# Kernel optimization log

Hardware: AMD Instinct MI355X
Metric: run time of the kernel (lower is better)

The kernel has to match this reference:

```python
import jax, jax.numpy as jnp
import numpy as np

B, T_ENC, FEAT, H, W2V, T_DEC, V = 32, 80, 4096, 256, 256, 30, 32000


def lstm_cell(x, h, c, w_ih, w_hh, b_ih, b_hh):
    # PyTorch LSTMCell: gates order i, f, g, o
    g = x @ w_ih.T + h @ w_hh.T + b_ih + b_hh
    i, f, gg, o = jnp.split(g, 4, axis=-1)
    c_new = jax.nn.sigmoid(f) * c + jax.nn.sigmoid(i) * jnp.tanh(gg)
    h_new = jax.nn.sigmoid(o) * jnp.tanh(c_new)
    return h_new, c_new


def setup_inputs() -> dict:
    key = jax.random.key(0)
    ks = jax.random.split(key, 13)
    s = 0.05
    return {
        'feat': jax.random.normal(ks[0], (B, T_ENC, FEAT), jnp.float32),
        'caption': jax.random.normal(ks[1], (B, T_DEC, W2V), jnp.float32),
        'caption_one_hot': jax.random.normal(ks[2], (B, T_DEC, V), jnp.float32),
        'keep_rate': 1,
        'w_ih1': jax.random.normal(ks[3], (4 * H, FEAT), jnp.float32) * s,
        'w_hh1': jax.random.normal(ks[4], (4 * H, H), jnp.float32) * s,
        'b_ih1': jax.random.normal(ks[5], (4 * H,), jnp.float32) * s,
        'b_hh1': jax.random.normal(ks[6], (4 * H,), jnp.float32) * s,
        'w_ih2': jax.random.normal(ks[7], (4 * H, H + W2V), jnp.float32) * s,
        'w_hh2': jax.random.normal(ks[8], (4 * H, H), jnp.float32) * s,
        'b_ih2': jax.random.normal(ks[9], (4 * H,), jnp.float32) * s,
        'b_hh2': jax.random.normal(ks[10], (4 * H,), jnp.float32) * s,
        'w_out': jax.random.normal(ks[11], (V, H), jnp.float32) * s,
        'b_out': jax.random.normal(ks[12], (V,), jnp.float32) * s,
    }


def reference(feat, caption, caption_one_hot, keep_rate,
              w_ih1, w_hh1, b_ih1, b_hh1,
              w_ih2, w_hh2, b_ih2, b_hh2,
              w_out, b_out):
    zeros_h = jnp.zeros((B, H), feat.dtype)
    pad1 = jnp.zeros((B, FEAT), feat.dtype)

    # ---------------- encoder: 80 steps ----------------
    def enc_step(carry, x_t):
        h1, c1, h2, c2 = carry
        h1, c1 = lstm_cell(x_t, h1, c1, w_ih1, w_hh1, b_ih1, b_hh1)
        h2, c2 = lstm_cell(jnp.concatenate([zeros_h, h1], axis=1), h2, c2,
                           w_ih2, w_hh2, b_ih2, b_hh2)
        return (h1, c1, h2, c2), h2

    (h1, c1, h2, c2), enc_h2 = jax.lax.scan(
        enc_step, (zeros_h, zeros_h, zeros_h, zeros_h),
        jnp.transpose(feat, (1, 0, 2)))
    enc_h2 = jnp.transpose(enc_h2, (1, 0, 2))  # [B, 80, H]

    # ---------------- decoder: teacher forcing (coin>=100 never fires) ----
    targets = jnp.argmax(caption_one_hot, axis=-1)  # [B, T_DEC]

    def dec_step(carry, xs):
        h1, c1, h2, c2, loss = carry
        word_t, tgt_t = xs  # [B, W2V], [B]
        h1, c1 = lstm_cell(pad1, h1, c1, w_ih1, w_hh1, b_ih1, b_hh1)
        h2n, c2 = lstm_cell(jnp.concatenate([word_t, h1], axis=1), h2, c2,
                            w_ih2, w_hh2, b_ih2, b_hh2)
        logits = h2n @ w_out.T + b_out  # [B, V]
        logp = jax.nn.log_softmax(logits, axis=-1)
        ce = -jnp.take_along_axis(logp, tgt_t[:, None], axis=1)[:, 0]
        loss = loss + jnp.mean(ce) / B  # sum(mean-CE)/batch, per original
        # attention: scores of encoder h2 states against current h2
        attn = jax.nn.softmax(jnp.einsum('bsh,bh->bs', enc_h2, h2n), axis=-1)
        ctx = jnp.einsum('bs,bsh->bh', attn, enc_h2)  # replaces h2 for next step
        return (h1, c1, ctx, c2, loss), None

    xs = (jnp.transpose(caption[:, :T_DEC - 1, :], (1, 0, 2)),
          jnp.transpose(targets[:, 1:T_DEC], (1, 0)))
    (h1, c1, h2, c2, total_loss), _ = jax.lax.scan(
        dec_step, (h1, c1, h2, c2, jnp.float32(0.0)), xs)
    return total_loss
```

## Files before the change

kernel.cpp:

```cpp
#include <hip/hip_runtime.h>
#include <hip/hip_bf16.h>
#include <math.h>

#define BB 32
#define TE 80
#define FEAT 4096
#define HH 256
#define W2V 256
#define TD 30
#define VV 32000
#define G4 1024

typedef unsigned short u16;
typedef unsigned int u32;
using f32x4 = __attribute__((ext_vector_type(4))) float;
using bf16x8 = __attribute__((ext_vector_type(8))) short;
using f16x2 = __attribute__((ext_vector_type(2))) _Float16;

#define SENT 0xFFFFFFFFu

__device__ __forceinline__ float sigm(float x) { return 1.0f / (1.0f + expf(-x)); }
__device__ __forceinline__ u16 f2bf(float f) {
  u32 u = __float_as_uint(f);
  u32 r = (u + 0x7FFFu + ((u >> 16) & 1u)) >> 16;
  return (u16)r;
}
__device__ __forceinline__ u32 packh2(float lo, float hi) {
  f16x2 v = {(_Float16)lo, (_Float16)hi};
  return __builtin_bit_cast(u32, v);
}

#define AT_LOAD(p)     __hip_atomic_load((p), __ATOMIC_RELAXED, __HIP_MEMORY_SCOPE_AGENT)
#define AT_STORE(p, v) __hip_atomic_store((p), (v), __ATOMIC_RELAXED, __HIP_MEMORY_SCOPE_AGENT)

__device__ __forceinline__ float fdot2h(f16x2 a, f16x2 b, float c) {
#if __has_builtin(__builtin_amdgcn_fdot2)
  return __builtin_amdgcn_fdot2(a, b, c, false);
#else
  return c + (float)a[0] * (float)b[0] + (float)a[1] * (float)b[1];
#endif
}

__global__ __launch_bounds__(256) void prep_kernel(
    const float* __restrict__ w_ih1, const float* __restrict__ w_out,
    const float* __restrict__ w_ih2, const float* __restrict__ caption,
    const float* __restrict__ onehot,
    const float* __restrict__ b_ih1, const float* __restrict__ b_hh1,
    const float* __restrict__ b_ih2, const float* __restrict__ b_hh2,
    u16* __restrict__ w_ih1b, u16* __restrict__ wPK,
    u16* __restrict__ w_ih2lb, u16* __restrict__ capb,
    float* __restrict__ bias1, float* __restrict__ bias2,
    u32* __restrict__ H1H, u32* __restrict__ H2H,
    float* __restrict__ loss, int* __restrict__ cectr,
    int* __restrict__ targets) {
  int blk = blockIdx.x, tid = threadIdx.x;
  if (blk < 4096) {
    int i = blk * 256 + tid;
    float4 v = *(const float4*)&w_ih1[(size_t)i * 4];
    *(ushort4*)&w_ih1b[(size_t)i * 4] =
        make_ushort4(f2bf(v.x), f2bf(v.y), f2bf(v.z), f2bf(v.w));
  } else if (blk < 8096) {
    int i = (blk - 4096) * 256 + tid;
    int n = i >> 5, kg = i & 31;
    float4 v0 = *(const float4*)&w_out[(size_t)n * 256 + kg * 8];
    float4 v1 = *(const float4*)&w_out[(size_t)n * 256 + kg * 8 + 4];
    size_t dst = ((size_t)((n >> 4) * 32 + kg) * 16 + (n & 15)) * 8;
    *(ushort4*)&wPK[dst] = make_ushort4(f2bf(v0.x), f2bf(v0.y), f2bf(v0.z), f2bf(v0.w));
    *(ushort4*)&wPK[dst + 4] = make_ushort4(f2bf(v1.x), f2bf(v1.y), f2bf(v1.z), f2bf(v1.w));
  } else if (blk < 8352) {
    int i = (blk - 8096) * 256 + tid;
    int row = i >> 6, c = i & 63;
    float4 v = *(const float4*)&w_ih2[(size_t)row * 512 + c * 4];
    *(ushort4*)&w_ih2lb[(size_t)row * 256 + c * 4] =
        make_ushort4(f2bf(v.x), f2bf(v.y), f2bf(v.z), f2bf(v.w));
  } else if (blk < 8592) {
    int i = (blk - 8352) * 256 + tid;
    float4 v = *(const float4*)&caption[(size_t)i * 4];
    *(ushort4*)&capb[(size_t)i * 4] =
        make_ushort4(f2bf(v.x), f2bf(v.y), f2bf(v.z), f2bf(v.w));
  } else if (blk < 10352) {
    int i = (blk - 8592) * 256 + tid;
    u32 v = (i < 4096) ? 0u : SENT;
    H1H[i] = v;
    H2H[i] = v;
    if (i < 1024) {
      bias1[i] = b_ih1[i] + b_hh1[i];
      bias2[i] = b_ih2[i] + b_hh2[i];
    }
    if (i == 0) { *loss = 0.0f; *cectr = 0; }
  } else {
    int k = blk - 10352;
    int s = (k >> 5) + 1, b = k & 31;
    const float* row = &onehot[((size_t)b * TD + s) * VV];
    float bv = -INFINITY;
    int bi = 0x7fffffff;
    for (int v = tid; v < VV; v += 256) {
      float x = row[v];
      if (x > bv || (x == bv && v < bi)) { bv = x; bi = v; }
    }
    __shared__ float sv[256];
    __shared__ int si[256];
    sv[tid] = bv; si[tid] = bi;
    __syncthreads();
    for (int off = 128; off; off >>= 1) {
      if (tid < off) {
        float ov = sv[tid + off]; int oi = si[tid + off];
        if (ov > sv[tid] || (ov == sv[tid] && oi < si[tid])) { sv[tid] = ov; si[tid] = oi; }
      }
      __syncthreads();
    }
    if (tid == 0) targets[k] = si[0];
  }
}

#define GBM 128
#define GBN 128
#define GBK 64
#define LDSTR 72

__device__ void gemm_x1_body(char* smem, int bx, int by,
                             const float* __restrict__ A, const u16* __restrict__ Bw,
                             const float* __restrict__ bias, float* __restrict__ C) {
  u16* As = (u16*)smem;
  u16* Bs = (u16*)(smem + 18432);
  int tid = threadIdx.x;
  int rBase = by * GBM;
  int nBase = bx * GBN;
  int lane = tid & 63, w = tid >> 6;
  int wrow = (w >> 1) * 64, wcol = (w & 1) * 64;
  int lrow = lane & 15, lk = (lane >> 4) * 8;

  f32x4 acc[4][4];
#pragma unroll
  for (int m = 0; m < 4; ++m)
#pragma unroll
    for (int n = 0; n < 4; ++n) acc[m][n] = (f32x4){0.f, 0.f, 0.f, 0.f};

  for (int k0 = 0; k0 < FEAT; k0 += GBK) {
#pragma unroll
    for (int i = 0; i < 8; ++i) {
      int f = i * 256 + tid;
      int r = f >> 4, c = (f & 15) << 2;
      float4 v = *(const float4*)&A[(size_t)(rBase + r) * FEAT + k0 + c];
      *(ushort4*)&As[r * LDSTR + c] =
          make_ushort4(f2bf(v.x), f2bf(v.y), f2bf(v.z), f2bf(v.w));
    }
#pragma unroll
    for (int i = 0; i < 4; ++i) {
      int f = i * 256 + tid;
      int r = f >> 3, c = (f & 7) << 3;
      uint4 v = *(const uint4*)&Bw[(size_t)(nBase + r) * FEAT + k0 + c];
      *(uint4*)&Bs[r * LDSTR + c] = v;
    }
    __syncthreads();
#pragma unroll
    for (int s2 = 0; s2 < 2; ++s2) {
      bf16x8 af[4], bfr[4];
#pragma unroll
      for (int m = 0; m < 4; ++m)
        af[m] = *(const bf16x8*)&As[(wrow + m * 16 + lrow) * LDSTR + s2 * 32 + lk];
#pragma unroll
      for (int n = 0; n < 4; ++n)
        bfr[n] = *(const bf16x8*)&Bs[(wcol + n * 16 + lrow) * LDSTR + s2 * 32 + lk];
#pragma unroll
      for (int m = 0; m < 4; ++m)
#pragma unroll
        for (int n = 0; n < 4; ++n)
          acc[m][n] = __builtin_amdgcn_mfma_f32_16x16x32_bf16(
              af[m], bfr[n], acc[m][n], 0, 0, 0);
    }
    __syncthreads();
  }
  int orow = (lane >> 4) * 4;
  int ocol = lane & 15;
#pragma unroll
  for (int m = 0; m < 4; ++m)
#pragma unroll
    for (int n = 0; n < 4; ++n) {
      int cidx = nBase + wcol + n * 16 + ocol;
      float bv = bias[cidx];
#pragma unroll
      for (int q = 0; q < 4; ++q) {
        int r = rBase + wrow + m * 16 + orow + q;
        C[(size_t)r * G4 + cidx] = acc[m][n][q] + bv;
      }
    }
}

__device__ void xw2_body(char* smem, int nb, int t,
                         const u16* __restrict__ capb, const u16* __restrict__ w_ih2lb,
                         const float* __restrict__ bias2, float* __restrict__ XW2) {
  u16* As = (u16*)smem;
  u16* Bs = (u16*)(smem + 16896);
  int tid = threadIdx.x;
  int nBase = nb * 64;
#pragma unroll
  for (int it = 0; it < 4; ++it) {
    int i = it * 256 + tid;
    int r = i >> 5, c8 = i & 31;
    *(uint4*)&As[r * 264 + c8 * 8] =
        *(const uint4*)&capb[((size_t)r * TD + t) * 256 + c8 * 8];
  }
#pragma unroll
  for (int it = 0; it < 8; ++it) {
    int i = it * 256 + tid;
    int r = i >> 5, c8 = i & 31;
    *(uint4*)&Bs[r * 264 + c8 * 8] =
        *(const uint4*)&w_ih2lb[(size_t)(nBase + r) * 256 + c8 * 8];
  }
  __syncthreads();
  int lane = tid & 63, w = tid >> 6;
  int lrow = lane & 15, lk = (lane >> 4) * 8;
  f32x4 acc[2];
  acc[0] = (f32x4){0.f, 0.f, 0.f, 0.f};
  acc[1] = (f32x4){0.f, 0.f, 0.f, 0.f};
#pragma unroll
  for (int ks = 0; ks < 8; ++ks) {
    bf16x8 bfr = *(const bf16x8*)&Bs[(w * 16 + lrow) * 264 + ks * 32 + lk];
#pragma unroll
    for (int m = 0; m < 2; ++m) {
      bf16x8 af = *(const bf16x8*)&As[(m * 16 + lrow) * 264 + ks * 32 + lk];
      acc[m] = __builtin_amdgcn_mfma_f32_16x16x32_bf16(af, bfr, acc[m], 0, 0, 0);
    }
  }
  int col = nBase + w * 16 + (lane & 15);
  float bv = bias2[col];
  int orow = (lane >> 4) * 4;
#pragma unroll
  for (int m = 0; m < 2; ++m)
#pragma unroll
    for (int q = 0; q < 4; ++q) {
      int bb = m * 16 + orow + q;
      XW2[((size_t)t * 32 + bb) * G4 + col] = acc[m][q] + bv;
    }
}

__global__ __launch_bounds__(256) void gemms_kernel(
    const float* __restrict__ feat, const u16* __restrict__ w_ih1b,
    const float* __restrict__ bias1, float* __restrict__ X1,
    const u16* __restrict__ capb, const u16* __restrict__ w_ih2lb,
    const float* __restrict__ bias2, float* __restrict__ XW2) {
  __shared__ __align__(16) char smem[50688];
  int blk = blockIdx.x;
  if (blk < 160) {
    gemm_x1_body(smem, blk & 7, blk >> 3, feat, w_ih1b, bias1, X1);
  } else {
    int k = blk - 160;
    xw2_body(smem, k & 15, k >> 4, capb, w_ih2lb, bias2, XW2);
  }
}

struct RP {
  const float *X1, *XW2, *bias1, *bias2;
  const float *w_hh1, *w_ih2, *w_hh2;
  u32* H1H;
  u32* H2H;
  u16* H2NB;
};

__global__ __launch_bounds__(512, 1) void recurrent_kernel(RP p) {
  __shared__ float encL[TE][257];
  __shared__ __align__(16) f16x2 h1S[128], h2S[128];
  __shared__ float tmp2[256];
  __shared__ float gb[256];
  __shared__ float hnew[64];
  __shared__ float sc[80];
  __shared__ float red[4];
  int bid = blockIdx.x, tid = threadIdx.x;
  bool isL1 = bid < 128;
  int lb = isL1 ? bid : bid - 128;
  int b = lb >> 2, q = lb & 3;
  int r2 = tid >> 1, half = tid & 1;
  int g = r2 >> 6, jj = r2 & 63;
  int grow = (g << 8) + (q << 6) + jj;
  bool fin = (half == 0) && (r2 < 64);
  int jfin = (q << 6) + (r2 & 63);

  if (isL1) {
    f16x2 wA[64];
    {
      const float4* s4 = (const float4*)(p.w_hh1 + (size_t)grow * 256 + half * 128);
#pragma unroll
      for (int k = 0; k < 32; ++k) {
        float4 v = s4[k];
        wA[k * 2 + 0] = f16x2{(_Float16)v.x, (_Float16)v.y};
        wA[k * 2 + 1] = f16x2{(_Float16)v.z, (_Float16)v.w};
      }
    }
    float c1 = 0.f;
    float b1v[4];
    if (fin) {
#pragma unroll
      for (int g2 = 0; g2 < 4; ++g2) b1v[g2] = p.bias1[g2 * 256 + jfin];
    }
    __syncthreads();
    for (int T = 0; T < 109; ++T) {
      float x1v[4];
      if (fin) {
        if (T < TE) {
          const float* xb = &p.X1[((size_t)b * TE + T) * G4 + jfin];
#pragma unroll
          for (int g2 = 0; g2 < 4; ++g2) x1v[g2] = xb[g2 * 256];
        } else {
#pragma unroll
          for (int g2 = 0; g2 < 4; ++g2) x1v[g2] = b1v[g2];
        }
      }
      if (tid < 128) {
        const u32* src = &p.H1H[((size_t)T * 32 + b) * 128 + tid];
        u32 v = AT_LOAD(src);
        int gd = 0;
        while (v == SENT && ++gd < (1 << 24)) {
          __builtin_amdgcn_s_sleep(1);
          v = AT_LOAD(src);
        }
        h1S[tid] = __builtin_bit_cast(f16x2, v);
      }
      __syncthreads();
      float a1 = 0.f;
      {
        const uint4* hv = ((const uint4*)h1S) + half * 16;
#pragma unroll
        for (int k = 0; k < 16; ++k) {
          uint4 uu = hv[k];
          a1 = fdot2h(__builtin_bit_cast(f16x2, uu.x), wA[k * 4 + 0], a1);
          a1 = fdot2h(__builtin_bit_cast(f16x2, uu.y), wA[k * 4 + 1], a1);
          a1 = fdot2h(__builtin_bit_cast(f16x2, uu.z), wA[k * 4 + 2], a1);
          a1 = fdot2h(__builtin_bit_cast(f16x2, uu.w), wA[k * 4 + 3], a1);
        }
      }
      a1 += __shfl_xor(a1, 1);
      if (half == 0) gb[r2] = a1;
      __syncthreads();
      if (fin) {
        int u = r2;
        float gi = gb[u] + x1v[0];
        float gf = gb[64 + u] + x1v[1];
        float gG = gb[128 + u] + x1v[2];
        float go = gb[192 + u] + x1v[3];
        c1 = sigm(gf) * c1 + sigm(gi) * tanhf(gG);
        hnew[u] = sigm(go) * tanhf(c1);
      }
      __syncthreads();
      if (tid < 32) {
        u32 pk = packh2(hnew[2 * tid], hnew[2 * tid + 1]);
        AT_STORE(&p.H1H[((size_t)(T + 1) * 32 + b) * 128 + (q << 5) + tid], pk);
      }
    }
  } else {
    f16x2 wB[64], wC[64];
    {
      const float4* sB = (const float4*)(p.w_ih2 + (size_t)grow * 512 + 256 + half * 128);
      const float4* sC = (const float4*)(p.w_hh2 + (size_t)grow * 256 + half * 128);
#pragma unroll
      for (int k = 0; k < 32; ++k) {
        float4 v = sB[k];
        wB[k * 2 + 0] = f16x2{(_Float16)v.x, (_Float16)v.y};
        wB[k * 2 + 1] = f16x2{(_Float16)v.z, (_Float16)v.w};
        float4 u = sC[k];
        wC[k * 2 + 0] = f16x2{(_Float16)u.x, (_Float16)u.y};
        wC[k * 2 + 1] = f16x2{(_Float16)u.z, (_Float16)u.w};
      }
    }
    float c2 = 0.f;
    float b2v[4];
    if (fin) {
#pragma unroll
      for (int g2 = 0; g2 < 4; ++g2) b2v[g2] = p.bias2[g2 * 256 + jfin];
    }
    __syncthreads();
    for (int U = 1; U <= 109; ++U) {
      float x2v[4];
      if (fin) {
        if (U <= TE) {
#pragma unroll
          for (int g2 = 0; g2 < 4; ++g2) x2v[g2] = b2v[g2];
        } else {
          const float* xb = &p.XW2[((size_t)(U - 81) * 32 + b) * G4 + jfin];
#pragma unroll
          for (int g2 = 0; g2 < 4; ++g2) x2v[g2] = xb[g2 * 256];
        }
      }
      if (tid < 128) {
        const u32* src = &p.H1H[((size_t)U * 32 + b) * 128 + tid];
        u32 v = AT_LOAD(src);
        int gd = 0;
        while (v == SENT && ++gd < (1 << 24)) {
          __builtin_amdgcn_s_sleep(1);
          v = AT_LOAD(src);
        }
        h1S[tid] = __builtin_bit_cast(f16x2, v);
      } else if (tid < 256) {
        int t2 = tid - 128;
        const u32* src = &p.H2H[((size_t)(U - 1) * 32 + b) * 128 + t2];
        u32 v = AT_LOAD(src);
        int gd = 0;
        while (v == SENT && ++gd < (1 << 24)) {
          __builtin_amdgcn_s_sleep(1);
          v = AT_LOAD(src);
        }
        f16x2 hp = __builtin_bit_cast(f16x2, v);
        h2S[t2] = hp;
        tmp2[2 * t2] = (float)hp[0];
        tmp2[2 * t2 + 1] = (float)hp[1];
      }
      __syncthreads();
      if (U <= 81) {
        if (U >= 2 && tid < 256) encL[U - 2][tid] = tmp2[tid];
      } else {
        float a = 0.f;
        if (tid < TE) {
          const float* e = &encL[tid][0];
#pragma unroll 8
          for (int k2 = 0; k2 < 256; ++k2) a += e[k2] * tmp2[k2];
        }
        float av = (tid < TE) ? a : -INFINITY;
#pragma unroll
        for (int d = 32; d; d >>= 1) av = fmaxf(av, __shfl_xor(av, d));
        if (tid == 0) red[0] = av;
        if (tid == 64) red[1] = av;
        __syncthreads();
        float m = fmaxf(red[0], red[1]);
        float e = (tid < TE) ? expf(a - m) : 0.f;
        float sv = e;
#pragma unroll
        for (int d = 32; d; d >>= 1) sv += __shfl_xor(sv, d);
        if (tid == 0) red[2] = sv;
        if (tid == 64) red[3] = sv;
        __syncthreads();
        float inv = 1.0f / (red[2] + red[3]);
        if (tid < TE) sc[tid] = e * inv;
        __syncthreads();
        if (tid < 256) {
          float acc = 0.f;
          for (int t2 = 0; t2 < TE; ++t2) acc += sc[t2] * encL[t2][tid];
          tmp2[tid] = acc;
        }
        __syncthreads();
        if (tid < 128)
          h2S[tid] = f16x2{(_Float16)tmp2[2 * tid], (_Float16)tmp2[2 * tid + 1]};
      }
      __syncthreads();
      float a2 = 0.f;
      {
        const uint4* h1v = ((const uint4*)h1S) + half * 16;
        const uint4* h2v = ((const uint4*)h2S) + half * 16;
#pragma unroll
        for (int k = 0; k < 16; ++k) {
          uint4 uu = h1v[k];
          a2 = fdot2h(__builtin_bit_cast(f16x2, uu.x), wB[k * 4 + 0], a2);
          a2 = fdot2h(__builtin_bit_cast(f16x2, uu.y), wB[k * 4 + 1], a2);
          a2 = fdot2h(__builtin_bit_cast(f16x2, uu.z), wB[k * 4 + 2], a2);
          a2 = fdot2h(__builtin_bit_cast(f16x2, uu.w), wB[k * 4 + 3], a2);
        }
#pragma unroll
        for (int k = 0; k < 16; ++k) {
          uint4 uu = h2v[k];
          a2 = fdot2h(__builtin_bit_cast(f16x2, uu.x), wC[k * 4 + 0], a2);
          a2 = fdot2h(__builtin_bit_cast(f16x2, uu.y), wC[k * 4 + 1], a2);
          a2 = fdot2h(__builtin_bit_cast(f16x2, uu.z), wC[k * 4 + 2], a2);
          a2 = fdot2h(__builtin_bit_cast(f16x2, uu.w), wC[k * 4 + 3], a2);
        }
      }
      a2 += __shfl_xor(a2, 1);
      if (half == 0) gb[r2] = a2;
      __syncthreads();
      if (fin) {
        int u = r2;
        float gi = gb[u] + x2v[0];
        float gf = gb[64 + u] + x2v[1];
        float gG = gb[128 + u] + x2v[2];
        float go = gb[192 + u] + x2v[3];
        c2 = sigm(gf) * c2 + sigm(gi) * tanhf(gG);
        float h = sigm(go) * tanhf(c2);
        hnew[u] = h;
        if (U >= 81)
          p.H2NB[((size_t)(U - 81) * 32 + b) * 256 + jfin] = f2bf(h);
      }
      __syncthreads();
      if (tid < 32) {
        u32 pk = packh2(hnew[2 * tid], hnew[2 * tid + 1]);
        AT_STORE(&p.H2H[((size_t)U * 32 + b) * 128 + (q << 5) + tid], pk);
      }
    }
  }
}

__global__ __launch_bounds__(256, 1) void logits_ce_kernel(
    const u16* __restrict__ H2NB, const u16* __restrict__ wPK,
    const float* __restrict__ b_out, const int* __restrict__ targets,
    float* __restrict__ pmaxA, float* __restrict__ psumA,
    float* __restrict__ tgtv) {
  __shared__ __align__(16) u16 bS[32768];
  __shared__ __align__(16) u16 aS[32 * 264];
  __shared__ int tS[32];
  int tid = threadIdx.x, bid = blockIdx.x;
  const u16* src = wPK + (size_t)bid * 32768;
  for (int i = tid; i < 4096; i += 256)
    *(uint4*)&bS[i * 8] = *(const uint4*)&src[i * 8];
  int wid = tid >> 6, lane = tid & 63, lcol = lane & 15, lk = lane >> 4;
  float bo[2];
#pragma unroll
  for (int n = 0; n < 2; ++n) bo[n] = b_out[(bid * 8 + wid * 2 + n) * 16 + lcol];

  for (int rg = 0; rg < 29; ++rg) {
    __syncthreads();
    for (int i = tid; i < 1024; i += 256) {
      int r = i >> 5, c8 = i & 31;
      *(uint4*)&aS[r * 264 + c8 * 8] =
          *(const uint4*)&H2NB[(size_t)rg * 8192 + r * 256 + c8 * 8];
    }
    if (tid < 32) tS[tid] = targets[rg * 32 + tid];
    __syncthreads();
    f32x4 acc[2][2];
#pragma unroll
    for (int m = 0; m < 2; ++m)
#pragma unroll
      for (int n = 0; n < 2; ++n) acc[m][n] = (f32x4){0.f, 0.f, 0.f, 0.f};
#pragma unroll
    for (int ks = 0; ks < 8; ++ks) {
      bf16x8 a0 = *(const bf16x8*)&aS[lcol * 264 + ks * 32 + lk * 8];
      bf16x8 a1 = *(const bf16x8*)&aS[(16 + lcol) * 264 + ks * 32 + lk * 8];
      bf16x8 b0 = *(const bf16x8*)&bS[(wid * 2) * 4096 + ((ks * 4 + lk) * 16 + lcol) * 8];
      bf16x8 b1 = *(const bf16x8*)&bS[(wid * 2 + 1) * 4096 + ((ks * 4 + lk) * 16 + lcol) * 8];
      acc[0][0] = __builtin_amdgcn_mfma_f32_16x16x32_bf16(a0, b0, acc[0][0], 0, 0, 0);
      acc[0][1] = __builtin_amdgcn_mfma_f32_16x16x32_bf16(a0, b1, acc[0][1], 0, 0, 0);
      acc[1][0] = __builtin_amdgcn_mfma_f32_16x16x32_bf16(a1, b0, acc[1][0], 0, 0, 0);
      acc[1][1] = __builtin_amdgcn_mfma_f32_16x16x32_bf16(a1, b1, acc[1][1], 0, 0, 0);
    }
    int nbase = (bid * 8 + wid * 2) * 16 + lcol;
#pragma unroll
    for (int m = 0; m < 2; ++m) {
      float pm[4], psv[4];
#pragma unroll
      for (int q = 0; q < 4; ++q) {
        float v0 = acc[m][0][q] + bo[0];
        float v1 = acc[m][1][q] + bo[1];
        int r = m * 16 + lk * 4 + q;
        int tg = tS[r];
        if (tg == nbase) tgtv[rg * 32 + r] = v0;
        if (tg == nbase + 16) tgtv[rg * 32 + r] = v1;
        float mx = fmaxf(v0, v1);
#pragma unroll
        for (int d = 1; d < 16; d <<= 1) mx = fmaxf(mx, __shfl_xor(mx, d));
        float e = expf(v0 - mx) + expf(v1 - mx);
#pragma unroll
        for (int d = 1; d < 16; d <<= 1) e += __shfl_xor(e, d);
        pm[q] = mx;
        psv[q] = e;
      }
      if (lcol == 0) {
        int chunk = bid * 4 + wid;
#pragma unroll
        for (int q = 0; q < 4; ++q) {
          int r2 = rg * 32 + m * 16 + lk * 4 + q;
          pmaxA[(size_t)r2 * 1000 + chunk] = pm[q];
          psumA[(size_t)r2 * 1000 + chunk] = psv[q];
        }
      }
    }
  }
}

__global__ __launch_bounds__(256) void ce_final_kernel(
    const float* __restrict__ pmaxA, const float* __restrict__ psumA,
    const float* __restrict__ tgtv, float* __restrict__ loss,
    int* __restrict__ cectr, float* __restrict__ out) {
  int row = blockIdx.x;
  int tid = threadIdx.x;
  const float* pm = pmaxA + (size_t)row * 1000;
  const float* psv = psumA + (size_t)row * 1000;
  __shared__ float sm[256];
  float m = -INFINITY;
  for (int c = tid; c < 1000; c += 256) m = fmaxf(m, pm[c]);
  sm[tid] = m;
  __syncthreads();
  for (int off = 128; off; off >>= 1) {
    if (tid < off) sm[tid] = fmaxf(sm[tid], sm[tid + off]);
    __syncthreads();
  }
  float M = sm[0];
  __syncthreads();
  float s = 0.f;
  for (int c = tid; c < 1000; c += 256) s += psv[c] * expf(pm[c] - M);
  sm[tid] = s;
  __syncthreads();
  for (int off = 128; off; off >>= 1) {
    if (tid < off) sm[tid] += sm[tid + off];
    __syncthreads();
  }
  if (tid == 0) {
    atomicAdd(loss, (M + logf(sm[0]) - tgtv[row]) * (1.0f / 1024.0f));
    asm volatile("s_waitcnt vmcnt(0)" ::: "memory");
    int old = __hip_atomic_fetch_add(cectr, 1, __ATOMIC_ACQ_REL, __HIP_MEMORY_SCOPE_AGENT);
    if (old == 927) out[0] = AT_LOAD(loss);
  }
}

extern "C" void kernel_launch(void* const* d_in, const int* in_sizes, int n_in,
                              void* d_out, int out_size, void* d_ws, size_t ws_size,
                              hipStream_t stream) {
  (void)in_sizes; (void)n_in; (void)out_size; (void)ws_size;
  const float* feat    = (const float*)d_in[0];
  const float* caption = (const float*)d_in[1];
  const float* onehot  = (const float*)d_in[2];
  const float* w_ih1   = (const float*)d_in[4];
  const float* w_hh1   = (const float*)d_in[5];
  const float* b_ih1   = (const float*)d_in[6];
  const float* b_hh1   = (const float*)d_in[7];
  const float* w_ih2   = (const float*)d_in[8];
  const float* w_hh2   = (const float*)d_in[9];
  const float* b_ih2   = (const float*)d_in[10];
  const float* b_hh2   = (const float*)d_in[11];
  const float* w_out   = (const float*)d_in[12];
  const float* b_out   = (const float*)d_in[13];

  char* p = (char*)d_ws;
  auto alloc = [&](size_t bytes) {
    char* r = p;
    p += (bytes + 255) & ~(size_t)255;
    return r;
  };
  float* X1      = (float*)alloc(2560ull * 1024 * 4);
  float* XW2     = (float*)alloc(29ull * 32 * 1024 * 4);
  float* bias1   = (float*)alloc(1024 * 4);
  float* bias2   = (float*)alloc(1024 * 4);
  u32*   H1H     = (u32*)alloc(110ull * 32 * 128 * 4);
  u32*   H2H     = (u32*)alloc(110ull * 32 * 128 * 4);
  u16*   H2NB    = (u16*)alloc(29ull * 8192 * 2);
  float* pmaxA   = (float*)alloc(928ull * 1000 * 4);
  float* psumA   = (float*)alloc(928ull * 1000 * 4);
  float* tgtv    = (float*)alloc(928 * 4);
  float* lossacc = (float*)alloc(256);
  int*   cectr   = (int*)alloc(256);
  int*   targets = (int*)alloc(29 * 32 * 4);
  u16*   w_ih1b  = (u16*)alloc(1024ull * 4096 * 2);
  u16*   w_ih2lb = (u16*)alloc(1024ull * 256 * 2);
  u16*   capb    = (u16*)alloc(32ull * 30 * 256 * 2);
  u16*   wPK     = (u16*)alloc(2000ull * 32 * 16 * 8 * 2);

  prep_kernel<<<11280, 256, 0, stream>>>(
      w_ih1, w_out, w_ih2, caption, onehot,
      b_ih1, b_hh1, b_ih2, b_hh2,
      w_ih1b, wPK, w_ih2lb, capb,
      bias1, bias2, H1H, H2H, lossacc, cectr, targets);
  gemms_kernel<<<624, 256, 0, stream>>>(feat, w_ih1b, bias1, X1,
                                        capb, w_ih2lb, bias2, XW2);

  RP rp;
  rp.X1 = X1; rp.XW2 = XW2; rp.bias1 = bias1; rp.bias2 = bias2;
  rp.w_hh1 = w_hh1; rp.w_ih2 = w_ih2; rp.w_hh2 = w_hh2;
  rp.H1H = H1H; rp.H2H = H2H; rp.H2NB = H2NB;
  void* args[] = {&rp};
  hipLaunchCooperativeKernel((const void*)recurrent_kernel, dim3(256), dim3(512),
                             args, 0, stream);

  logits_ce_kernel<<<250, 256, 0, stream>>>(H2NB, wPK, b_out, targets, pmaxA, psumA, tgtv);
  ce_final_kernel<<<928, 256, 0, stream>>>(pmaxA, psumA, tgtv, lossacc, cectr,
                                           (float*)d_out);
}
```

Before: 735.9 us.

## Move h1 projection into layer-1 blocks, pre-convert feat, fuse CE final into logits

Layer-1 blocks now also compute the h1·W_ih2 partial products and publish them through a NaN-sentinel buffer, so layer-2 blocks only do the h2 recurrence and wait on a single producer. The feat tensor is converted to bf16 in the prep kernel, so the X1 GEMM loads bf16 directly instead of converting on every tile. w_out packing moves into the logits kernel, and the separate CE-final kernel is replaced by a grid-wide spin barrier plus in-kernel reduction. This shortens the serial recurrence critical path and removes one launch and a prep pass, at the cost of a larger workspace, extra atomics, and spin-wait deadlock risk if not all 250 blocks are co-resident.

```diff
diff --git a/kernel.cpp b/kernel.cpp
--- a/kernel.cpp
+++ b/kernel.cpp
@@ -18,6 +18,7 @@
 using f16x2 = __attribute__((ext_vector_type(2))) _Float16;
 
 #define SENT 0xFFFFFFFFu
+#define NANF 0x7FC00000u
 
 __device__ __forceinline__ float sigm(float x) { return 1.0f / (1.0f + expf(-x)); }
 __device__ __forceinline__ u16 f2bf(float f) {
@@ -42,54 +43,20 @@
 }
 
 __global__ __launch_bounds__(256) void prep_kernel(
-    const float* __restrict__ w_ih1, const float* __restrict__ w_out,
+    const float* __restrict__ feat, const float* __restrict__ w_ih1,
     const float* __restrict__ w_ih2, const float* __restrict__ caption,
     const float* __restrict__ onehot,
     const float* __restrict__ b_ih1, const float* __restrict__ b_hh1,
     const float* __restrict__ b_ih2, const float* __restrict__ b_hh2,
-    u16* __restrict__ w_ih1b, u16* __restrict__ wPK,
+    u16* __restrict__ featb, u16* __restrict__ w_ih1b,
     u16* __restrict__ w_ih2lb, u16* __restrict__ capb,
     float* __restrict__ bias1, float* __restrict__ bias2,
-    u32* __restrict__ H1H, u32* __restrict__ H2H,
-    float* __restrict__ loss, int* __restrict__ cectr,
+    u32* __restrict__ H1H, u32* __restrict__ H2H, u32* __restrict__ A2P,
+    float* __restrict__ loss, int* __restrict__ ctrs,
     int* __restrict__ targets) {
   int blk = blockIdx.x, tid = threadIdx.x;
-  if (blk < 4096) {
-    int i = blk * 256 + tid;
-    float4 v = *(const float4*)&w_ih1[(size_t)i * 4];
-    *(ushort4*)&w_ih1b[(size_t)i * 4] =
-        make_ushort4(f2bf(v.x), f2bf(v.y), f2bf(v.z), f2bf(v.w));
-  } else if (blk < 8096) {
-    int i = (blk - 4096) * 256 + tid;
-    int n = i >> 5, kg = i & 31;
-    float4 v0 = *(const float4*)&w_out[(size_t)n * 256 + kg * 8];
-    float4 v1 = *(const float4*)&w_out[(size_t)n * 256 + kg * 8 + 4];
-    size_t dst = ((size_t)((n >> 4) * 32 + kg) * 16 + (n & 15)) * 8;
-    *(ushort4*)&wPK[dst] = make_ushort4(f2bf(v0.x), f2bf(v0.y), f2bf(v0.z), f2bf(v0.w));
-    *(ushort4*)&wPK[dst + 4] = make_ushort4(f2bf(v1.x), f2bf(v1.y), f2bf(v1.z), f2bf(v1.w));
-  } else if (blk < 8352) {
-    int i = (blk - 8096) * 256 + tid;
-    int row = i >> 6, c = i & 63;
-    float4 v = *(const float4*)&w_ih2[(size_t)row * 512 + c * 4];
-    *(ushort4*)&w_ih2lb[(size_t)row * 256 + c * 4] =
-        make_ushort4(f2bf(v.x), f2bf(v.y), f2bf(v.z), f2bf(v.w));
-  } else if (blk < 8592) {
-    int i = (blk - 8352) * 256 + tid;
-    float4 v = *(const float4*)&caption[(size_t)i * 4];
-    *(ushort4*)&capb[(size_t)i * 4] =
-        make_ushort4(f2bf(v.x), f2bf(v.y), f2bf(v.z), f2bf(v.w));
-  } else if (blk < 10352) {
-    int i = (blk - 8592) * 256 + tid;
-    u32 v = (i < 4096) ? 0u : SENT;
-    H1H[i] = v;
-    H2H[i] = v;
-    if (i < 1024) {
-      bias1[i] = b_ih1[i] + b_hh1[i];
-      bias2[i] = b_ih2[i] + b_hh2[i];
-    }
-    if (i == 0) { *loss = 0.0f; *cectr = 0; }
-  } else {
-    int k = blk - 10352;
+  if (blk < 928) {
+    int k = blk;
     int s = (k >> 5) + 1, b = k & 31;
     const float* row = &onehot[((size_t)b * TD + s) * VV];
     float bv = -INFINITY;
@@ -110,6 +77,61 @@
       __syncthreads();
     }
     if (tid == 0) targets[k] = si[0];
+  } else if (blk < 3488) {
+    int i0 = (blk - 928) * 1024 + tid;
+#pragma unroll
+    for (int ii = 0; ii < 4; ++ii) {
+      int i = i0 + ii * 256;
+      float4 v = *(const float4*)&feat[(size_t)i * 4];
+      *(ushort4*)&featb[(size_t)i * 4] =
+          make_ushort4(f2bf(v.x), f2bf(v.y), f2bf(v.z), f2bf(v.w));
+    }
+  } else if (blk < 4512) {
+    int i0 = (blk - 3488) * 1024 + tid;
+#pragma unroll
+    for (int ii = 0; ii < 4; ++ii) {
+      int i = i0 + ii * 256;
+      float4 v = *(const float4*)&w_ih1[(size_t)i * 4];
+      *(ushort4*)&w_ih1b[(size_t)i * 4] =
+          make_ushort4(f2bf(v.x), f2bf(v.y), f2bf(v.z), f2bf(v.w));
+    }
+  } else if (blk < 4576) {
+    int i0 = (blk - 4512) * 1024 + tid;
+#pragma unroll
+    for (int ii = 0; ii < 4; ++ii) {
+      int i = i0 + ii * 256;
+      int row = i >> 6, c = (i & 63) * 4;
+      float4 v = *(const float4*)&w_ih2[(size_t)row * 512 + c];
+      *(ushort4*)&w_ih2lb[(size_t)row * 256 + c] =
+          make_ushort4(f2bf(v.x), f2bf(v.y), f2bf(v.z), f2bf(v.w));
+    }
+  } else if (blk < 4636) {
+    int i0 = (blk - 4576) * 1024 + tid;
+#pragma unroll
+    for (int ii = 0; ii < 4; ++ii) {
+      int i = i0 + ii * 256;
+      float4 v = *(const float4*)&caption[(size_t)i * 4];
+      *(ushort4*)&capb[(size_t)i * 4] =
+          make_ushort4(f2bf(v.x), f2bf(v.y), f2bf(v.z), f2bf(v.w));
+    }
+  } else if (blk < 5076) {
+    int i = (blk - 4636) * 256 + tid;
+    uint4 z = {0u, 0u, 0u, 0u};
+    uint4 s = {SENT, SENT, SENT, SENT};
+    uint4 v = (i < 1024) ? z : s;
+    ((uint4*)H1H)[i] = v;
+    ((uint4*)H2H)[i] = v;
+  } else if (blk < 5956) {
+    int i0 = (blk - 5076) * 1024 + tid;
+    uint4 s = {NANF, NANF, NANF, NANF};
+#pragma unroll
+    for (int ii = 0; ii < 4; ++ii) ((uint4*)A2P)[i0 + ii * 256] = s;
+  } else {
+    for (int i = tid; i < 1024; i += 256) {
+      bias1[i] = b_ih1[i] + b_hh1[i];
+      bias2[i] = b_ih2[i] + b_hh2[i];
+    }
+    if (tid == 0) { *loss = 0.0f; ctrs[0] = 0; ctrs[32] = 0; }
   }
 }
 
@@ -119,7 +141,7 @@
 #define LDSTR 72
 
 __device__ void gemm_x1_body(char* smem, int bx, int by,
-                             const float* __restrict__ A, const u16* __restrict__ Bw,
+                             const u16* __restrict__ Ab, const u16* __restrict__ Bw,
                              const float* __restrict__ bias, float* __restrict__ C) {
   u16* As = (u16*)smem;
   u16* Bs = (u16*)(smem + 18432);
@@ -138,19 +160,18 @@
 
   for (int k0 = 0; k0 < FEAT; k0 += GBK) {
 #pragma unroll
-    for (int i = 0; i < 8; ++i) {
-      int f = i * 256 + tid;
-      int r = f >> 4, c = (f & 15) << 2;
-      float4 v = *(const float4*)&A[(size_t)(rBase + r) * FEAT + k0 + c];
-      *(ushort4*)&As[r * LDSTR + c] =
-          make_ushort4(f2bf(v.x), f2bf(v.y), f2bf(v.z), f2bf(v.w));
-    }
-#pragma unroll
     for (int i = 0; i < 4; ++i) {
       int f = i * 256 + tid;
-      int r = f >> 3, c = (f & 7) << 3;
-      uint4 v = *(const uint4*)&Bw[(size_t)(nBase + r) * FEAT + k0 + c];
-      *(uint4*)&Bs[r * LDSTR + c] = v;
+      int r = f >> 3, c8 = f & 7;
+      *(uint4*)&As[r * LDSTR + c8 * 8] =
+          *(const uint4*)&Ab[(size_t)(rBase + r) * FEAT + k0 + c8 * 8];
+    }
+#pragma unroll
+    for (int i = 0; i < 4; ++i) {
+      int f = i * 256 + tid;
+      int r = f >> 3, c8 = f & 7;
+      *(uint4*)&Bs[r * LDSTR + c8 * 8] =
+          *(const uint4*)&Bw[(size_t)(nBase + r) * FEAT + k0 + c8 * 8];
     }
     __syncthreads();
 #pragma unroll
@@ -236,14 +257,14 @@
 }
 
 __global__ __launch_bounds__(256) void gemms_kernel(
-    const float* __restrict__ feat, const u16* __restrict__ w_ih1b,
+    const u16* __restrict__ featb, const u16* __restrict__ w_ih1b,
     const float* __restrict__ bias1, float* __restrict__ X1,
     const u16* __restrict__ capb, const u16* __restrict__ w_ih2lb,
     const float* __restrict__ bias2, float* __restrict__ XW2) {
   __shared__ __align__(16) char smem[50688];
   int blk = blockIdx.x;
   if (blk < 160) {
-    gemm_x1_body(smem, blk & 7, blk >> 3, feat, w_ih1b, bias1, X1);
+    gemm_x1_body(smem, blk & 7, blk >> 3, featb, w_ih1b, bias1, X1);
   } else {
     int k = blk - 160;
     xw2_body(smem, k & 15, k >> 4, capb, w_ih2lb, bias2, XW2);
@@ -255,14 +276,16 @@
   const float *w_hh1, *w_ih2, *w_hh2;
   u32* H1H;
   u32* H2H;
+  u32* A2P;
   u16* H2NB;
 };
 
 __global__ __launch_bounds__(512, 1) void recurrent_kernel(RP p) {
   __shared__ float encL[TE][257];
-  __shared__ __align__(16) f16x2 h1S[128], h2S[128];
+  __shared__ __align__(16) f16x2 hS[128];
   __shared__ float tmp2[256];
   __shared__ float gb[256];
+  __shared__ float a2pS[256];
   __shared__ float hnew[64];
   __shared__ float sc[80];
   __shared__ float red[4];
@@ -273,38 +296,34 @@
   int r2 = tid >> 1, half = tid & 1;
   int g = r2 >> 6, jj = r2 & 63;
   int grow = (g << 8) + (q << 6) + jj;
-  bool fin = (half == 0) && (r2 < 64);
-  int jfin = (q << 6) + (r2 & 63);
+  int jf = (q << 6) + tid;
 
   if (isL1) {
-    f16x2 wA[64];
+    f16x2 wA[64], wB[64];
     {
-      const float4* s4 = (const float4*)(p.w_hh1 + (size_t)grow * 256 + half * 128);
+      const float4* sA = (const float4*)(p.w_hh1 + (size_t)grow * 256 + half * 128);
+      const float4* sB = (const float4*)(p.w_ih2 + (size_t)grow * 512 + 256 + half * 128);
 #pragma unroll
       for (int k = 0; k < 32; ++k) {
-        float4 v = s4[k];
+        float4 v = sA[k];
         wA[k * 2 + 0] = f16x2{(_Float16)v.x, (_Float16)v.y};
         wA[k * 2 + 1] = f16x2{(_Float16)v.z, (_Float16)v.w};
+        float4 u = sB[k];
+        wB[k * 2 + 0] = f16x2{(_Float16)u.x, (_Float16)u.y};
+        wB[k * 2 + 1] = f16x2{(_Float16)u.z, (_Float16)u.w};
       }
     }
     float c1 = 0.f;
-    float b1v[4];
-    if (fin) {
-#pragma unroll
-      for (int g2 = 0; g2 < 4; ++g2) b1v[g2] = p.bias1[g2 * 256 + jfin];
-    }
-    __syncthreads();
-    for (int T = 0; T < 109; ++T) {
-      float x1v[4];
-      if (fin) {
-        if (T < TE) {
-          const float* xb = &p.X1[((size_t)b * TE + T) * G4 + jfin];
-#pragma unroll
-          for (int g2 = 0; g2 < 4; ++g2) x1v[g2] = xb[g2 * 256];
-        } else {
-#pragma unroll
-          for (int g2 = 0; g2 < 4; ++g2) x1v[g2] = b1v[g2];
-        }
+    float b1v0 = 0, b1v1 = 0, b1v2 = 0, b1v3 = 0;
+    if (tid < 64) {
+      b1v0 = p.bias1[jf]; b1v1 = p.bias1[256 + jf];
+      b1v2 = p.bias1[512 + jf]; b1v3 = p.bias1[768 + jf];
+    }
+    for (int T = 0; T <= 109; ++T) {
+      float x0 = b1v0, x1 = b1v1, x2 = b1v2, x3 = b1v3;
+      if (tid < 64 && T < TE) {
+        const float* xb = &p.X1[((size_t)b * TE + T) * G4 + jf];
+        x0 = xb[0]; x1 = xb[256]; x2 = xb[512]; x3 = xb[768];
       }
       if (tid < 128) {
         const u32* src = &p.H1H[((size_t)T * 32 + b) * 128 + tid];
@@ -314,97 +333,100 @@
           __builtin_amdgcn_s_sleep(1);
           v = AT_LOAD(src);
         }
-        h1S[tid] = __builtin_bit_cast(f16x2, v);
-      }
-      __syncthreads();
-      float a1 = 0.f;
+        hS[tid] = __builtin_bit_cast(f16x2, v);
+      }
+      __syncthreads();
+      float a1 = 0.f, a2 = 0.f;
       {
-        const uint4* hv = ((const uint4*)h1S) + half * 16;
+        const uint4* hv = ((const uint4*)hS) + half * 16;
 #pragma unroll
         for (int k = 0; k < 16; ++k) {
           uint4 uu = hv[k];
-          a1 = fdot2h(__builtin_bit_cast(f16x2, uu.x), wA[k * 4 + 0], a1);
-          a1 = fdot2h(__builtin_bit_cast(f16x2, uu.y), wA[k * 4 + 1], a1);
-          a1 = fdot2h(__builtin_bit_cast(f16x2, uu.z), wA[k * 4 + 2], a1);
-          a1 = fdot2h(__builtin_bit_cast(f16x2, uu.w), wA[k * 4 + 3], a1);
+          f16x2 e0 = __builtin_bit_cast(f16x2, uu.x), e1 = __builtin_bit_cast(f16x2, uu.y);
+          f16x2 e2 = __builtin_bit_cast(f16x2, uu.z), e3 = __builtin_bit_cast(f16x2, uu.w);
+          a1 = fdot2h(e0, wA[k * 4 + 0], a1);
+          a2 = fdot2h(e0, wB[k * 4 + 0], a2);
+          a1 = fdot2h(e1, wA[k * 4 + 1], a1);
+          a2 = fdot2h(e1, wB[k * 4 + 1], a2);
+          a1 = fdot2h(e2, wA[k * 4 + 2], a1);
+          a2 = fdot2h(e2, wB[k * 4 + 2], a2);
+          a1 = fdot2h(e3, wA[k * 4 + 3], a1);
+          a2 = fdot2h(e3, wB[k * 4 + 3], a2);
         }
       }
       a1 += __shfl_xor(a1, 1);
-      if (half == 0) gb[r2] = a1;
-      __syncthreads();
-      if (fin) {
-        int u = r2;
-        float gi = gb[u] + x1v[0];
-        float gf = gb[64 + u] + x1v[1];
-        float gG = gb[128 + u] + x1v[2];
-        float go = gb[192 + u] + x1v[3];
-        c1 = sigm(gf) * c1 + sigm(gi) * tanhf(gG);
-        hnew[u] = sigm(go) * tanhf(c1);
-      }
-      __syncthreads();
-      if (tid < 32) {
-        u32 pk = packh2(hnew[2 * tid], hnew[2 * tid + 1]);
-        AT_STORE(&p.H1H[((size_t)(T + 1) * 32 + b) * 128 + (q << 5) + tid], pk);
+      a2 += __shfl_xor(a2, 1);
+      if (half == 0) {
+        gb[r2] = a1;
+        if (T >= 1)
+          AT_STORE(&p.A2P[((size_t)T * 32 + b) * 1024 + grow], __float_as_uint(a2));
+      }
+      __syncthreads();
+      if (T <= 108) {
+        if (tid < 64) {
+          float gi = gb[tid] + x0;
+          float gf = gb[64 + tid] + x1;
+          float gG = gb[128 + tid] + x2;
+          float go = gb[192 + tid] + x3;
+          c1 = sigm(gf) * c1 + sigm(gi) * tanhf(gG);
+          hnew[tid] = sigm(go) * tanhf(c1);
+        }
+        if (tid < 32) {
+          u32 pk = packh2(hnew[2 * tid], hnew[2 * tid + 1]);
+          AT_STORE(&p.H1H[((size_t)(T + 1) * 32 + b) * 128 + (q << 5) + tid], pk);
+        }
       }
     }
   } else {
-    f16x2 wB[64], wC[64];
+    f16x2 wC[64];
     {
-      const float4* sB = (const float4*)(p.w_ih2 + (size_t)grow * 512 + 256 + half * 128);
       const float4* sC = (const float4*)(p.w_hh2 + (size_t)grow * 256 + half * 128);
 #pragma unroll
       for (int k = 0; k < 32; ++k) {
-        float4 v = sB[k];
-        wB[k * 2 + 0] = f16x2{(_Float16)v.x, (_Float16)v.y};
-        wB[k * 2 + 1] = f16x2{(_Float16)v.z, (_Float16)v.w};
         float4 u = sC[k];
         wC[k * 2 + 0] = f16x2{(_Float16)u.x, (_Float16)u.y};
         wC[k * 2 + 1] = f16x2{(_Float16)u.z, (_Float16)u.w};
       }
     }
     float c2 = 0.f;
-    float b2v[4];
-    if (fin) {
-#pragma unroll
-      for (int g2 = 0; g2 < 4; ++g2) b2v[g2] = p.bias2[g2 * 256 + jfin];
-    }
-    __syncthreads();
+    float b2v0 = 0, b2v1 = 0, b2v2 = 0, b2v3 = 0;
+    if (tid < 64) {
+      b2v0 = p.bias2[jf]; b2v1 = p.bias2[256 + jf];
+      b2v2 = p.bias2[512 + jf]; b2v3 = p.bias2[768 + jf];
+    }
     for (int U = 1; U <= 109; ++U) {
-      float x2v[4];
-      if (fin) {
-        if (U <= TE) {
-#pragma unroll
-          for (int g2 = 0; g2 < 4; ++g2) x2v[g2] = b2v[g2];
-        } else {
-          const float* xb = &p.XW2[((size_t)(U - 81) * 32 + b) * G4 + jfin];
-#pragma unroll
-          for (int g2 = 0; g2 < 4; ++g2) x2v[g2] = xb[g2 * 256];
-        }
+      float x0 = b2v0, x1 = b2v1, x2 = b2v2, x3 = b2v3;
+      if (tid < 64 && U >= 81) {
+        const float* xb = &p.XW2[((size_t)(U - 81) * 32 + b) * G4 + jf];
+        x0 = xb[0]; x1 = xb[256]; x2 = xb[512]; x3 = xb[768];
       }
       if (tid < 128) {
-        const u32* src = &p.H1H[((size_t)U * 32 + b) * 128 + tid];
+        const u32* src = &p.H2H[((size_t)(U - 1) * 32 + b) * 128 + tid];
         u32 v = AT_LOAD(src);
         int gd = 0;
-        while (v == SENT && ++gd < (1 << 24)) {
+        while (v == SENT && ++gd < (1 << 26)) v = AT_LOAD(src);
+        f16x2 hp = __builtin_bit_cast(f16x2, v);
+        hS[tid] = hp;
+        tmp2[2 * tid] = (float)hp[0];
+        tmp2[2 * tid + 1] = (float)hp[1];
+      } else if (tid < 384) {
+        int rr = tid - 128;
+        int growp = ((rr >> 6) << 8) + (q << 6) + (rr & 63);
+        const u32* src = &p.A2P[((size_t)U * 32 + b) * 1024 + growp];
+        u32 v = AT_LOAD(src);
+        int gd = 0;
+        while (v == NANF && ++gd < (1 << 24)) {
           __builtin_amdgcn_s_sleep(1);
           v = AT_LOAD(src);
         }
-        h1S[tid] = __builtin_bit_cast(f16x2, v);
-      } else if (tid < 256) {
-        int t2 = tid - 128;
-        const u32* src = &p.H2H[((size_t)(U - 1) * 32 + b) * 128 + t2];
-        u32 v = AT_LOAD(src);
-        int gd = 0;
-        while (v == SENT && ++gd < (1 << 24)) {
-          __builtin_amdgcn_s_sleep(1);
-          v = AT_LOAD(src);
-        }
-        f16x2 hp = __builtin_bit_cast(f16x2, v);
-        h2S[t2] = hp;
-        tmp2[2 * t2] = (float)hp[0];
-        tmp2[2 * t2 + 1] = (float)hp[1];
-      }
-      __syncthreads();
+        a2pS[rr] = __uint_as_float(v);
+      }
+      __syncthreads();
+      float a2p0 = 0, a2p1 = 0, a2p2 = 0, a2p3 = 0;
+      if (tid < 64) {
+        a2p0 = a2pS[tid]; a2p1 = a2pS[64 + tid];
+        a2p2 = a2pS[128 + tid]; a2p3 = a2pS[192 + tid];
+      }
       if (U <= 81) {
         if (U >= 2 && tid < 256) encL[U - 2][tid] = tmp2[tid];
       } else {
@@ -421,15 +443,15 @@
         if (tid == 64) red[1] = av;
         __syncthreads();
         float m = fmaxf(red[0], red[1]);
-        float e = (tid < TE) ? expf(a - m) : 0.f;
-        float sv = e;
+        float e2 = (tid < TE) ? expf(a - m) : 0.f;
+        float sv = e2;
 #pragma unroll
         for (int d = 32; d; d >>= 1) sv += __shfl_xor(sv, d);
         if (tid == 0) red[2] = sv;
         if (tid == 64) red[3] = sv;
         __syncthreads();
         float inv = 1.0f / (red[2] + red[3]);
-        if (tid < TE) sc[tid] = e * inv;
+        if (tid < TE) sc[tid] = e2 * inv;
         __syncthreads();
         if (tid < 256) {
           float acc = 0.f;
@@ -438,24 +460,15 @@
         }
         __syncthreads();
         if (tid < 128)
-          h2S[tid] = f16x2{(_Float16)tmp2[2 * tid], (_Float16)tmp2[2 * tid + 1]};
-      }
-      __syncthreads();
+          hS[tid] = f16x2{(_Float16)tmp2[2 * tid], (_Float16)tmp2[2 * tid + 1]};
+        __syncthreads();
+      }
       float a2 = 0.f;
       {
-        const uint4* h1v = ((const uint4*)h1S) + half * 16;
-        const uint4* h2v = ((const uint4*)h2S) + half * 16;
+        const uint4* hv = ((const uint4*)hS) + half * 16;
 #pragma unroll
         for (int k = 0; k < 16; ++k) {
-          uint4 uu = h1v[k];
-          a2 = fdot2h(__builtin_bit_cast(f16x2, uu.x), wB[k * 4 + 0], a2);
-          a2 = fdot2h(__builtin_bit_cast(f16x2, uu.y), wB[k * 4 + 1], a2);
-          a2 = fdot2h(__builtin_bit_cast(f16x2, uu.z), wB[k * 4 + 2], a2);
-          a2 = fdot2h(__builtin_bit_cast(f16x2, uu.w), wB[k * 4 + 3], a2);
-        }
-#pragma unroll
-        for (int k = 0; k < 16; ++k) {
-          uint4 uu = h2v[k];
+          uint4 uu = hv[k];
           a2 = fdot2h(__builtin_bit_cast(f16x2, uu.x), wC[k * 4 + 0], a2);
           a2 = fdot2h(__builtin_bit_cast(f16x2, uu.y), wC[k * 4 + 1], a2);
           a2 = fdot2h(__builtin_bit_cast(f16x2, uu.z), wC[k * 4 + 2], a2);
@@ -465,19 +478,17 @@
       a2 += __shfl_xor(a2, 1);
       if (half == 0) gb[r2] = a2;
       __syncthreads();
-      if (fin) {
-        int u = r2;
-        float gi = gb[u] + x2v[0];
-        float gf = gb[64 + u] + x2v[1];
-        float gG = gb[128 + u] + x2v[2];
-        float go = gb[192 + u] + x2v[3];
+      if (tid < 64) {
+        float gi = gb[tid] + a2p0 + x0;
+        float gf = gb[64 + tid] + a2p1 + x1;
+        float gG = gb[128 + tid] + a2p2 + x2;
+        float go = gb[192 + tid] + a2p3 + x3;
         c2 = sigm(gf) * c2 + sigm(gi) * tanhf(gG);
         float h = sigm(go) * tanhf(c2);
-        hnew[u] = h;
+        hnew[tid] = h;
         if (U >= 81)
-          p.H2NB[((size_t)(U - 81) * 32 + b) * 256 + jfin] = f2bf(h);
-      }
-      __syncthreads();
+          p.H2NB[((size_t)(U - 81) * 32 + b) * 256 + jf] = f2bf(h);
+      }
       if (tid < 32) {
         u32 pk = packh2(hnew[2 * tid], hnew[2 * tid + 1]);
         AT_STORE(&p.H2H[((size_t)U * 32 + b) * 128 + (q << 5) + tid], pk);
@@ -486,18 +497,28 @@
   }
 }
 
-__global__ __launch_bounds__(256, 1) void logits_ce_kernel(
-    const u16* __restrict__ H2NB, const u16* __restrict__ wPK,
+__global__ __launch_bounds__(256, 1) void logits_final_kernel(
+    const u16* __restrict__ H2NB, const float* __restrict__ w_out,
     const float* __restrict__ b_out, const int* __restrict__ targets,
-    float* __restrict__ pmaxA, float* __restrict__ psumA,
-    float* __restrict__ tgtv) {
+    u32* __restrict__ pmaxA, u32* __restrict__ psumA, u32* __restrict__ tgtv,
+    float* __restrict__ loss, int* __restrict__ ctrs, float* __restrict__ out) {
   __shared__ __align__(16) u16 bS[32768];
   __shared__ __align__(16) u16 aS[32 * 264];
   __shared__ int tS[32];
+  __shared__ float sm[256];
   int tid = threadIdx.x, bid = blockIdx.x;
-  const u16* src = wPK + (size_t)bid * 32768;
-  for (int i = tid; i < 4096; i += 256)
-    *(uint4*)&bS[i * 8] = *(const uint4*)&src[i * 8];
+#pragma unroll
+  for (int it = 0; it < 16; ++it) {
+    int id = it * 256 + tid;
+    int nt = id >> 9, rr = (id >> 5) & 15, kg = id & 31;
+    int n = bid * 128 + nt * 16 + rr;
+    const float* src = &w_out[(size_t)n * 256 + kg * 8];
+    float4 v0 = *(const float4*)src;
+    float4 v1 = *(const float4*)(src + 4);
+    u16* dst = &bS[(size_t)((nt * 32 + kg) * 16 + rr) * 8];
+    *(ushort4*)dst = make_ushort4(f2bf(v0.x), f2bf(v0.y), f2bf(v0.z), f2bf(v0.w));
+    *(ushort4*)(dst + 4) = make_ushort4(f2bf(v1.x), f2bf(v1.y), f2bf(v1.z), f2bf(v1.w));
+  }
   int wid = tid >> 6, lane = tid & 63, lcol = lane & 15, lk = lane >> 4;
   float bo[2];
 #pragma unroll
@@ -533,67 +554,79 @@
     for (int m = 0; m < 2; ++m) {
       float pm[4], psv[4];
 #pragma unroll
-      for (int q = 0; q < 4; ++q) {
-        float v0 = acc[m][0][q] + bo[0];
-        float v1 = acc[m][1][q] + bo[1];
-        int r = m * 16 + lk * 4 + q;
+      for (int qq = 0; qq < 4; ++qq) {
+        float v0 = acc[m][0][qq] + bo[0];
+        float v1 = acc[m][1][qq] + bo[1];
+        int r = m * 16 + lk * 4 + qq;
         int tg = tS[r];
-        if (tg == nbase) tgtv[rg * 32 + r] = v0;
-        if (tg == nbase + 16) tgtv[rg * 32 + r] = v1;
+        if (tg == nbase) AT_STORE(&tgtv[rg * 32 + r], __float_as_uint(v0));
+        if (tg == nbase + 16) AT_STORE(&tgtv[rg * 32 + r], __float_as_uint(v1));
         float mx = fmaxf(v0, v1);
 #pragma unroll
         for (int d = 1; d < 16; d <<= 1) mx = fmaxf(mx, __shfl_xor(mx, d));
         float e = expf(v0 - mx) + expf(v1 - mx);
 #pragma unroll
         for (int d = 1; d < 16; d <<= 1) e += __shfl_xor(e, d);
-        pm[q] = mx;
-        psv[q] = e;
+        pm[qq] = mx;
+        psv[qq] = e;
       }
       if (lcol == 0) {
         int chunk = bid * 4 + wid;
 #pragma unroll
-        for (int q = 0; q < 4; ++q) {
-          int r2 = rg * 32 + m * 16 + lk * 4 + q;
-          pmaxA[(size_t)r2 * 1000 + chunk] = pm[q];
-          psumA[(size_t)r2 * 1000 + chunk] = psv[q];
-        }
-      }
-    }
-  }
-}
-
-__global__ __launch_bounds__(256) void ce_final_kernel(
-    const float* __restrict__ pmaxA, const float* __restrict__ psumA,
-    const float* __restrict__ tgtv, float* __restrict__ loss,
-    int* __restrict__ cectr, float* __restrict__ out) {
-  int row = blockIdx.x;
-  int tid = threadIdx.x;
-  const float* pm = pmaxA + (size_t)row * 1000;
-  const float* psv = psumA + (size_t)row * 1000;
-  __shared__ float sm[256];
-  float m = -INFINITY;
-  for (int c = tid; c < 1000; c += 256) m = fmaxf(m, pm[c]);
-  sm[tid] = m;
+        for (int qq = 0; qq < 4; ++qq) {
+          int r2 = rg * 32 + m * 16 + lk * 4 + qq;
+          AT_STORE(&pmaxA[(size_t)r2 * 1000 + chunk], __float_as_uint(pm[qq]));
+          AT_STORE(&psumA[(size_t)r2 * 1000 + chunk], __float_as_uint(psv[qq]));
+        }
+      }
+    }
+  }
+  asm volatile("s_waitcnt vmcnt(0)" ::: "memory");
   __syncthreads();
-  for (int off = 128; off; off >>= 1) {
-    if (tid < off) sm[tid] = fmaxf(sm[tid], sm[tid + off]);
-    __syncthreads();
-  }
-  float M = sm[0];
+  if (tid == 0) {
+    __hip_atomic_fetch_add(&ctrs[0], 1, __ATOMIC_RELEASE, __HIP_MEMORY_SCOPE_AGENT);
+    int gd = 0;
+    while (__hip_atomic_load(&ctrs[0], __ATOMIC_ACQUIRE, __HIP_MEMORY_SCOPE_AGENT) < 250 &&
+           ++gd < (1 << 26))
+      __builtin_amdgcn_s_sleep(2);
+  }
   __syncthreads();
-  float s = 0.f;
-  for (int c = tid; c < 1000; c += 256) s += psv[c] * expf(pm[c] - M);
-  sm[tid] = s;
-  __syncthreads();
-  for (int off = 128; off; off >>= 1) {
-    if (tid < off) sm[tid] += sm[tid + off];
-    __syncthreads();
-  }
+#pragma unroll
+  for (int k = 0; k < 4; ++k) {
+    int row = bid * 4 + k;
+    if (row < 928) {
+      const u32* pm = pmaxA + (size_t)row * 1000;
+      const u32* psv = psumA + (size_t)row * 1000;
+      float m = -INFINITY;
+      for (int c = tid; c < 1000; c += 256) m = fmaxf(m, __uint_as_float(AT_LOAD(&pm[c])));
+      sm[tid] = m;
+      __syncthreads();
+      for (int off = 128; off; off >>= 1) {
+        if (tid < off) sm[tid] = fmaxf(sm[tid], sm[tid + off]);
+        __syncthreads();
+      }
+      float M = sm[0];
+      __syncthreads();
+      float s = 0.f;
+      for (int c = tid; c < 1000; c += 256)
+        s += __uint_as_float(AT_LOAD(&psv[c])) * expf(__uint_as_float(AT_LOAD(&pm[c])) - M);
+      sm[tid] = s;
+      __syncthreads();
+      for (int off = 128; off; off >>= 1) {
+        if (tid < off) sm[tid] += sm[tid + off];
+        __syncthreads();
+      }
+      if (tid == 0) {
+        float tv = __uint_as_float(AT_LOAD(&tgtv[row]));
+        atomicAdd(loss, (M + logf(sm[0]) - tv) * (1.0f / 1024.0f));
+      }
+      __syncthreads();
+    }
+  }
+  asm volatile("s_waitcnt vmcnt(0)" ::: "memory");
   if (tid == 0) {
-    atomicAdd(loss, (M + logf(sm[0]) - tgtv[row]) * (1.0f / 1024.0f));
-    asm volatile("s_waitcnt vmcnt(0)" ::: "memory");
-    int old = __hip_atomic_fetch_add(cectr, 1, __ATOMIC_ACQ_REL, __HIP_MEMORY_SCOPE_AGENT);
-    if (old == 927) out[0] = AT_LOAD(loss);
+    int old = __hip_atomic_fetch_add(&ctrs[32], 1, __ATOMIC_ACQ_REL, __HIP_MEMORY_SCOPE_AGENT);
+    if (old == 249) out[0] = __uint_as_float(AT_LOAD((u32*)loss));
   }
 }
 
@@ -627,35 +660,36 @@
   float* bias2   = (float*)alloc(1024 * 4);
   u32*   H1H     = (u32*)alloc(110ull * 32 * 128 * 4);
   u32*   H2H     = (u32*)alloc(110ull * 32 * 128 * 4);
+  u32*   A2P     = (u32*)alloc(110ull * 32 * 1024 * 4);
   u16*   H2NB    = (u16*)alloc(29ull * 8192 * 2);
-  float* pmaxA   = (float*)alloc(928ull * 1000 * 4);
-  float* psumA   = (float*)alloc(928ull * 1000 * 4);
-  float* tgtv    = (float*)alloc(928 * 4);
+  u32*   pmaxA   = (u32*)alloc(928ull * 1000 * 4);
+  u32*   psumA   = (u32*)alloc(928ull * 1000 * 4);
+  u32*   tgtv    = (u32*)alloc(928 * 4);
   float* lossacc = (float*)alloc(256);
-  int*   cectr   = (int*)alloc(256);
+  int*   ctrs    = (int*)alloc(256);
   int*   targets = (int*)alloc(29 * 32 * 4);
+  u16*   featb   = (u16*)alloc(2560ull * 4096 * 2);
   u16*   w_ih1b  = (u16*)alloc(1024ull * 4096 * 2);
   u16*   w_ih2lb = (u16*)alloc(1024ull * 256 * 2);
   u16*   capb    = (u16*)alloc(32ull * 30 * 256 * 2);
-  u16*   wPK     = (u16*)alloc(2000ull * 32 * 16 * 8 * 2);
-
-  prep_kernel<<<11280, 256, 0, stream>>>(
-      w_ih1, w_out, w_ih2, caption, onehot,
+
+  prep_kernel<<<5957, 256, 0, stream>>>(
+      feat, w_ih1, w_ih2, caption, onehot,
       b_ih1, b_hh1, b_ih2, b_hh2,
-      w_ih1b, wPK, w_ih2lb, capb,
-      bias1, bias2, H1H, H2H, lossacc, cectr, targets);
-  gemms_kernel<<<624, 256, 0, stream>>>(feat, w_ih1b, bias1, X1,
+      featb, w_ih1b, w_ih2lb, capb,
+      bias1, bias2, H1H, H2H, A2P, lossacc, ctrs, targets);
+  gemms_kernel<<<624, 256, 0, stream>>>(featb, w_ih1b, bias1, X1,
                                         capb, w_ih2lb, bias2, XW2);
 
   RP rp;
   rp.X1 = X1; rp.XW2 = XW2; rp.bias1 = bias1; rp.bias2 = bias2;
   rp.w_hh1 = w_hh1; rp.w_ih2 = w_ih2; rp.w_hh2 = w_hh2;
-  rp.H1H = H1H; rp.H2H = H2H; rp.H2NB = H2NB;
+  rp.H1H = H1H; rp.H2H = H2H; rp.A2P = A2P; rp.H2NB = H2NB;
   void* args[] = {&rp};
   hipLaunchCooperativeKernel((const void*)recurrent_kernel, dim3(256), dim3(512),
                              args, 0, stream);
 
-  logits_ce_kernel<<<250, 256, 0, stream>>>(H2NB, wPK, b_out, targets, pmaxA, psumA, tgtv);
-  ce_final_kernel<<<928, 256, 0, stream>>>(pmaxA, psumA, tgtv, lossacc, cectr,
-                                           (float*)d_out);
-}
+  logits_final_kernel<<<250, 256, 0, stream>>>(H2NB, w_out, b_out, targets,
+                                               pmaxA, psumA, tgtv, lossacc, ctrs,
+                                               (float*)d_out);
+}
```

New measurement: 687.5 us. 1.07x faster.
